# Kernel optimization log

Measured on AMD Instinct MI355X. Metric: run time of the kernel, lower is better.

The kernel has to match this reference:

```python
import jax, jax.numpy as jnp
import numpy as np

EPS = 1e-5
QMAX = 127.0


def fake_quant_int8(x):
    """Per-tensor symmetric int8 fake-quant (quantize+dequantize), dynamic scale.
    Mirrors brevitas Int8ActPerTensorFloat / Int8WeightPerTensorFloat math."""
    scale = jnp.maximum(jnp.max(jnp.abs(x)) / QMAX, 1e-8)
    q = jnp.clip(jnp.round(x / scale), -128.0, 127.0) * scale
    # straight-through estimator (identity grad through quant)
    return x + jax.lax.stop_gradient(q - x)


def layer_norm(x, g, b):
    mu = jnp.mean(x, axis=-1, keepdims=True)
    var = jnp.mean(jnp.square(x - mu), axis=-1, keepdims=True)
    return (x - mu) * jax.lax.rsqrt(var + EPS) * g + b


def setup_inputs() -> dict:
    key = jax.random.key(0)
    B, S, D, H = 64, 196, 768, 12
    M = 4 * D
    ks = jax.random.split(key, 8)
    s = lambda d: 1.0 / np.sqrt(d)
    return {
        "x": jax.random.normal(ks[0], (B, S, D), jnp.float32),
        "ln1_g": jnp.ones((D,), jnp.float32),
        "ln1_b": jnp.zeros((D,), jnp.float32),
        "ln2_g": jnp.ones((D,), jnp.float32),
        "ln2_b": jnp.zeros((D,), jnp.float32),
        "w_qkv": jax.random.normal(ks[1], (D, 3 * D), jnp.float32) * s(D),
        "b_qkv": jnp.zeros((3 * D,), jnp.float32),
        "w_o": jax.random.normal(ks[2], (D, D), jnp.float32) * s(D),
        "b_o": jnp.zeros((D,), jnp.float32),
        "w1": jax.random.normal(ks[3], (D, M), jnp.float32) * s(D),
        "b1": jnp.zeros((M,), jnp.float32),
        "w2": jax.random.normal(ks[4], (M, D), jnp.float32) * s(M),
        "b2": jnp.zeros((D,), jnp.float32),
    }


def _block(x, ln1_g, ln1_b, ln2_g, ln2_b, w_qkv, b_qkv, w_o, b_o, w1, b1, w2, b2):
    B, S, D = x.shape
    H = 12
    hd = D // H

    # --- LN -> quant -> MHSA -> add ---
    r1 = x
    h = fake_quant_int8(layer_norm(x, ln1_g, ln1_b))
    qkv = jnp.einsum("bsd,de->bse", h, fake_quant_int8(w_qkv)) + b_qkv
    q, k, v = jnp.split(qkv, 3, axis=-1)
    q = q.reshape(B, S, H, hd)
    k = k.reshape(B, S, H, hd)
    v = v.reshape(B, S, H, hd)
    logits = jnp.einsum("bqhd,bkhd->bhqk", q, k) / jnp.sqrt(jnp.float32(hd))
    attn = jax.nn.softmax(logits, axis=-1)
    ctx = jnp.einsum("bhqk,bkhd->bqhd", attn, v).reshape(B, S, D)
    ctx = fake_quant_int8(ctx)
    mhsa = jnp.einsum("bsd,de->bse", ctx, fake_quant_int8(w_o)) + b_o
    x = mhsa + r1

    # --- LN -> quant -> MLP (fc1 -> GELU -> quant -> fc2) -> add ---
    r2 = x
    h = fake_quant_int8(layer_norm(x, ln2_g, ln2_b))
    h = jnp.einsum("bsd,dm->bsm", h, fake_quant_int8(w1)) + b1
    h = jax.nn.gelu(h, approximate=False)  # torch nn.GELU default = exact erf
    h = fake_quant_int8(h)
    h = jnp.einsum("bsm,md->bsd", h, fake_quant_int8(w2)) + b2
    return h + r2


def reference(x, ln1_g, ln1_b, ln2_g, ln2_b, w_qkv, b_qkv, w_o, b_o, w1, b1, w2, b2):
    return _block(x, ln1_g, ln1_b, ln2_g, ln2_b, w_qkv, b_qkv, w_o, b_o, w1, b1, w2, b2)
```

## Files before the change

### kernel.cpp

```cpp
#include <hip/hip_runtime.h>
#include <cstdint>
#include <cstddef>

#define DEVFN __device__ __forceinline__

typedef short bf16x8 __attribute__((ext_vector_type(8)));
typedef float f32x4  __attribute__((ext_vector_type(4)));
typedef int   i32x4  __attribute__((ext_vector_type(4)));

static constexpr int NTOK  = 64 * 196;
static constexpr int DMODEL= 768;
static constexpr int NHEAD = 12;
static constexpr int NQKV  = 2304;
static constexpr int MMLP  = 3072;
static constexpr int SEQ   = 196;
static constexpr int NBATCH= 64;

enum { SL_LN1=0, SL_WQKV=1, SL_CTX=2, SL_WO=3, SL_LN2=4, SL_W1=5, SL_GELU=6, SL_W2=7 };

static constexpr int NSH       = 64;
static constexpr int SH_STRIDE = 64;
static constexpr int SLOTS_U32 = NSH * SH_STRIDE;

DEVFN float bf2f(unsigned short u){ return __uint_as_float(((unsigned)u) << 16); }
DEVFN unsigned short f2bf(float f){
  unsigned u = __float_as_uint(f);
  u += 0x7fffu + ((u >> 16) & 1u);
  return (unsigned short)(u >> 16);
}
DEVFN void split_bf(float v, unsigned short& hi, unsigned short& lo){
  hi = f2bf(v);
  lo = f2bf(v - bf2f(hi));
}
DEVFN float slot_absmax(const unsigned* __restrict__ slots, int slot){
  unsigned m = 0u;
#pragma unroll
  for (int j = 0; j < NSH; j++){
    unsigned u = slots[j * SH_STRIDE + slot];
    m = (u > m) ? u : m;
  }
  return __uint_as_float(m);
}
DEVFN float slot_scale(const unsigned* __restrict__ slots, int slot){
  return fmaxf(slot_absmax(slots, slot) / 127.0f, 1e-8f);
}
DEVFN void scatter_amax(unsigned* slots, int slot, unsigned bucket, float v){
  atomicMax(slots + (bucket & (NSH - 1)) * SH_STRIDE + slot, __float_as_uint(v));
}
DEVFN float quantval(float x, float s){
  float q = rintf(x / s);
  return fminf(fmaxf(q, -128.0f), 127.0f);
}
DEVFN unsigned pack4(float a, float b, float c, float d){
  return  ((unsigned)(unsigned char)(char)(int)a)
        | ((unsigned)(unsigned char)(char)(int)b << 8)
        | ((unsigned)(unsigned char)(char)(int)c << 16)
        | ((unsigned)(unsigned char)(char)(int)d << 24);
}
DEVFN float gelu_fast(float v){
  float s  = v * 0.70710678118654752f;
  float ax = fabsf(s);
  float t  = __builtin_amdgcn_rcpf(fmaf(0.3275911f, ax, 1.0f));
  float p  = t * fmaf(t, fmaf(t, fmaf(t, fmaf(t, 1.061405429f, -1.453152027f),
                                      1.421413741f), -0.284496736f), 0.254829592f);
  float er = fmaf(-p, __expf(-ax * ax), 1.0f);
  unsigned sgn = __float_as_uint(s) & 0x80000000u;
  er = __uint_as_float(__float_as_uint(er) | sgn);
  return 0.5f * v * (1.0f + er);
}
DEVFN f32x4 mfma16(bf16x8 a, bf16x8 b, f32x4 c){
  return __builtin_amdgcn_mfma_f32_16x16x32_bf16(a, b, c, 0, 0, 0);
}
DEVFN i32x4 mfma16i8(i32x4 a, i32x4 b, i32x4 c){
  return __builtin_amdgcn_mfma_i32_16x16x64_i8(a, b, c, 0, 0, 0);
}
DEVFN void async_ld16(const void* g, void* lds){
  __builtin_amdgcn_global_load_lds((const __attribute__((address_space(1))) void*)g,
                                   (__attribute__((address_space(3))) void*)lds, 16, 0, 0);
}
DEVFN int vidx(int d, int s){
  return d * 256 + (s ^ (((d ^ (d >> 2)) & 7) << 3));
}

__global__ void k_init(unsigned* slots){
  int i = blockIdx.x * blockDim.x + threadIdx.x;
  if (i < SLOTS_U32) slots[i] = 0u;
}

__global__ void k_absmax4(const float* __restrict__ x0, const float* __restrict__ x1,
                          const float* __restrict__ x2, const float* __restrict__ x3,
                          unsigned* slots){
  int bid = blockIdx.x;
  const float* x; int n4, slot, b0, nb;
  if (bid < 256)      { x = x0; n4 = DMODEL * NQKV  / 4; slot = SL_WQKV; b0 = 0;   nb = 256; }
  else if (bid < 384) { x = x1; n4 = DMODEL * DMODEL/ 4; slot = SL_WO;   b0 = 256; nb = 128; }
  else if (bid < 640) { x = x2; n4 = DMODEL * MMLP  / 4; slot = SL_W1;   b0 = 384; nb = 256; }
  else                { x = x3; n4 = MMLP   * DMODEL/ 4; slot = SL_W2;   b0 = 640; nb = 256; }
  int lb = bid - b0;
  float m = 0.f;
  const float4* x4 = (const float4*)x;
  int stride = nb * blockDim.x;
  for (int j = lb * blockDim.x + threadIdx.x; j < n4; j += stride){
    float4 v = x4[j];
    m = fmaxf(m, fmaxf(fmaxf(fabsf(v.x), fabsf(v.y)), fmaxf(fabsf(v.z), fabsf(v.w))));
  }
  for (int off = 32; off; off >>= 1) m = fmaxf(m, __shfl_xor(m, off));
  __shared__ float wm[4];
  int lane = threadIdx.x & 63, w = threadIdx.x >> 6;
  if (lane == 0) wm[w] = m;
  __syncthreads();
  if (threadIdx.x == 0){
    float bm = fmaxf(fmaxf(wm[0], wm[1]), fmaxf(wm[2], wm[3]));
    scatter_amax(slots, slot, bid, bm);
  }
}

__global__ void k_quant_transpose4(const float* __restrict__ w0, const float* __restrict__ w1,
                                   const float* __restrict__ w2, const float* __restrict__ w3,
                                   char* __restrict__ t0, char* __restrict__ t1,
                                   char* __restrict__ t2, char* __restrict__ t3,
                                   const unsigned* __restrict__ slots){
  int bid = blockIdx.x;
  const float* w; char* wt; int K, N, slot, lb;
  if (bid < 1728)      { w = w0; wt = t0; K = DMODEL; N = NQKV;   slot = SL_WQKV; lb = bid; }
  else if (bid < 2304) { w = w1; wt = t1; K = DMODEL; N = DMODEL; slot = SL_WO;   lb = bid - 1728; }
  else if (bid < 4608) { w = w2; wt = t2; K = DMODEL; N = MMLP;   slot = SL_W1;   lb = bid - 2304; }
  else                 { w = w3; wt = t3; K = MMLP;   N = DMODEL; slot = SL_W2;   lb = bid - 4608; }
  int nx = N / 32;
  int bx = lb % nx, by = lb / nx;

  __shared__ float tile[32][33];
  float s = slot_scale(slots, slot);
  int n0 = bx * 32, k0 = by * 32;
  int tx = threadIdx.x & 31, ty = threadIdx.x >> 5;
#pragma unroll
  for (int i = 0; i < 4; i++){
    int k = k0 + ty + i * 8;
    float v = w[(size_t)k * N + n0 + tx];
    tile[ty + i * 8][tx] = quantval(v, s);
  }
  __syncthreads();
  int n = threadIdx.x >> 3, kg = threadIdx.x & 7;
  unsigned o = pack4(tile[kg * 4 + 0][n], tile[kg * 4 + 1][n],
                     tile[kg * 4 + 2][n], tile[kg * 4 + 3][n]);
  *(unsigned*)(wt + (size_t)(n0 + n) * K + k0 + kg * 4) = o;
}

__global__ void k_layernorm(const float* __restrict__ x, const float* __restrict__ g,
                            const float* __restrict__ b, float* __restrict__ out,
                            unsigned* slots, int slot){
  int w = threadIdx.x >> 6, lane = threadIdx.x & 63;
  int row = blockIdx.x * 4 + w;
  const float4* xr = (const float4*)(x + (size_t)row * DMODEL);
  float4 v[3];
  float sum = 0.f;
#pragma unroll
  for (int i = 0; i < 3; i++){ v[i] = xr[i * 64 + lane]; sum += v[i].x + v[i].y + v[i].z + v[i].w; }
  for (int off = 32; off; off >>= 1) sum += __shfl_xor(sum, off);
  float mu = sum * (1.0f / 768.0f);
  float vs = 0.f;
#pragma unroll
  for (int i = 0; i < 3; i++){
    float dx = v[i].x - mu, dy = v[i].y - mu, dz = v[i].z - mu, dw = v[i].w - mu;
    vs += dx * dx + dy * dy + dz * dz + dw * dw;
  }
  for (int off = 32; off; off >>= 1) vs += __shfl_xor(vs, off);
  float inv = 1.0f / sqrtf(vs * (1.0f / 768.0f) + 1e-5f);
  const float4* g4 = (const float4*)g; const float4* b4 = (const float4*)b;
  float4* o4 = (float4*)(out + (size_t)row * DMODEL);
  float am = 0.f;
#pragma unroll
  for (int i = 0; i < 3; i++){
    float4 gg = g4[i * 64 + lane], bb = b4[i * 64 + lane], o;
    o.x = (v[i].x - mu) * inv * gg.x + bb.x;
    o.y = (v[i].y - mu) * inv * gg.y + bb.y;
    o.z = (v[i].z - mu) * inv * gg.z + bb.z;
    o.w = (v[i].w - mu) * inv * gg.w + bb.w;
    am = fmaxf(am, fmaxf(fmaxf(fabsf(o.x), fabsf(o.y)), fmaxf(fabsf(o.z), fabsf(o.w))));
    o4[i * 64 + lane] = o;
  }
  for (int off = 32; off; off >>= 1) am = fmaxf(am, __shfl_xor(am, off));
  __shared__ float am4[4];
  if (lane == 0) am4[w] = am;
  __syncthreads();
  if (threadIdx.x == 0){
    float bm = fmaxf(fmaxf(am4[0], am4[1]), fmaxf(am4[2], am4[3]));
    scatter_amax(slots, slot, blockIdx.x, bm);
  }
}

__global__ void k_quant_act(const float* __restrict__ x, unsigned* __restrict__ out,
                            int n4, const unsigned* __restrict__ slots, int slot){
  float s = slot_scale(slots, slot);
  const float4* x4 = (const float4*)x;
  int stride = gridDim.x * blockDim.x;
  for (int j = blockIdx.x * blockDim.x + threadIdx.x; j < n4; j += stride){
    float4 v = x4[j];
    out[j] = pack4(quantval(v.x, s), quantval(v.y, s), quantval(v.z, s), quantval(v.w, s));
  }
}

__global__ void k_quant_bf16_i8(const unsigned short* __restrict__ x, unsigned* __restrict__ out,
                                int n4, const unsigned* __restrict__ slots, int slot){
  float s = slot_scale(slots, slot);
  const ushort4* x4 = (const ushort4*)x;
  int stride = gridDim.x * blockDim.x;
  for (int j = blockIdx.x * blockDim.x + threadIdx.x; j < n4; j += stride){
    ushort4 v = x4[j];
    out[j] = pack4(quantval(bf2f(v.x), s), quantval(bf2f(v.y), s),
                   quantval(bf2f(v.z), s), quantval(bf2f(v.w), s));
  }
}

template<int EPI>
__launch_bounds__(256, 4)
__global__ void k_gemm(const char* __restrict__ A,
                       const char* __restrict__ Bt,
                       const float* __restrict__ bias,
                       const float* __restrict__ res,
                       float* __restrict__ Cf,
                       unsigned short* __restrict__ Cb,
                       const unsigned* __restrict__ slots, int sa_slot, int sb_slot,
                       unsigned* gmax_slots, int gmax_slot,
                       int M, int N, int K)
{
  __shared__ __align__(16) char smem[32768];
  __shared__ float gm4[4];
  const int tid  = threadIdx.x;
  const int lane = tid & 63;
  const int wv   = tid >> 6;
  const int wx   = wv & 1, wy = wv >> 1;
  const int quad = lane >> 4;
  const int l16  = lane & 15;
  const int m0 = blockIdx.y * 128, n0 = blockIdx.x * 128;

  auto issue = [&](int k0, int buf){
#pragma unroll
    for (int i = 0; i < 2; i++){
      int c = tid + i * 256;
      int row = c >> 2, q = c & 3;
      int qs = (q - ((row + (row >> 2)) & 3)) & 3;
      async_ld16(A + (size_t)(m0 + row) * K + k0 + qs * 16,
                 smem + buf * 8192 + (i * 256 + wv * 64) * 16);
    }
#pragma unroll
    for (int i = 0; i < 2; i++){
      int c = tid + i * 256;
      int row = c >> 2, q = c & 3;
      int qs = (q - ((row + (row >> 2)) & 3)) & 3;
      async_ld16(Bt + (size_t)(n0 + row) * K + k0 + qs * 16,
                 smem + 16384 + buf * 8192 + (i * 256 + wv * 64) * 16);
    }
  };

  i32x4 acc[4][4] = {};
  const int nk = K >> 6;
  issue(0, 0);

  const int ch = (((quad + (l16 & 3) + (l16 >> 2)) & 3)) * 16;

  for (int k = 0; k < nk; k++){
    const int cur = k & 1;
    if (k + 1 < nk){
      issue((k + 1) << 6, cur ^ 1);
      asm volatile("s_waitcnt vmcnt(4)" ::: "memory");
    } else {
      asm volatile("s_waitcnt vmcnt(0)" ::: "memory");
    }
    asm volatile("s_barrier" ::: "memory");

    const char* Ab = smem + cur * 8192;
    const char* Bb = smem + 16384 + cur * 8192;
    i32x4 af[4], bfr[4];
#pragma unroll
    for (int i = 0; i < 4; i++)
      af[i] = *(const i32x4*)(Ab + (wy * 64 + i * 16 + l16) * 64 + ch);
#pragma unroll
    for (int j = 0; j < 4; j++)
      bfr[j] = *(const i32x4*)(Bb + (wx * 64 + j * 16 + l16) * 64 + ch);
    asm volatile("s_waitcnt lgkmcnt(0)" ::: "memory");
    asm volatile("s_barrier" ::: "memory");

#pragma unroll
    for (int i = 0; i < 4; i++)
#pragma unroll
      for (int j = 0; j < 4; j++)
        acc[i][j] = mfma16i8(af[i], bfr[j], acc[i][j]);
  }
  __syncthreads();

  float (*stage)[132] = (float (*)[132])smem;
  const float sc = slot_scale(slots, sa_slot) * slot_scale(slots, sb_slot);
  const int col4 = (tid & 31) * 4;
  const int gc   = n0 + col4;
  const float4 bb = *(const float4*)&bias[gc];
  float gmax = 0.f;
#pragma unroll
  for (int i = 0; i < 4; i++){
#pragma unroll
    for (int j = 0; j < 4; j++)
#pragma unroll
      for (int r = 0; r < 4; r++)
        stage[wy * 16 + quad * 4 + r][wx * 64 + j * 16 + l16] = (float)acc[i][j][r];
    __syncthreads();
#pragma unroll
    for (int rr = 0; rr < 4; rr++){
      const int rl = rr * 8 + (tid >> 5);
      const int gm = m0 + ((rl >> 4) * 64) + i * 16 + (rl & 15);
      float4 v = *(const float4*)&stage[rl][col4];
      v.x = v.x * sc + bb.x; v.y = v.y * sc + bb.y;
      v.z = v.z * sc + bb.z; v.w = v.w * sc + bb.w;
      if constexpr (EPI == 1){
        float4 rv = *(const float4*)&res[(size_t)gm * N + gc];
        v.x += rv.x; v.y += rv.y; v.z += rv.z; v.w += rv.w;
        *(float4*)&Cf[(size_t)gm * N + gc] = v;
      } else if constexpr (EPI == 2){
        float g0 = gelu_fast(v.x);
        float g1 = gelu_fast(v.y);
        float g2 = gelu_fast(v.z);
        float g3 = gelu_fast(v.w);
        gmax = fmaxf(gmax, fmaxf(fmaxf(fabsf(g0), fabsf(g1)), fmaxf(fabsf(g2), fabsf(g3))));
        ushort4 o = {f2bf(g0), f2bf(g1), f2bf(g2), f2bf(g3)};
        *(ushort4*)&Cb[(size_t)gm * N + gc] = o;
      } else {
        *(float4*)&Cf[(size_t)gm * N + gc] = v;
      }
    }
    __syncthreads();
  }
  if constexpr (EPI == 2){
    for (int off = 32; off; off >>= 1) gmax = fmaxf(gmax, __shfl_xor(gmax, off));
    if (lane == 0) gm4[wv] = gmax;
    __syncthreads();
    if (tid == 0){
      float bm = fmaxf(fmaxf(gm4[0], gm4[1]), fmaxf(gm4[2], gm4[3]));
      scatter_amax(gmax_slots, gmax_slot, blockIdx.x + blockIdx.y * gridDim.x, bm);
    }
  }
}

__launch_bounds__(832, 4)
__global__ void k_attention(const float* __restrict__ qkv, float* __restrict__ ctx,
                            unsigned* slots){
  __shared__ __align__(16) unsigned short Khi[208 * 72], Klo[208 * 72];
  __shared__ __align__(16) unsigned short Vhi[64 * 256], Vlo[64 * 256];
  __shared__ __align__(16) unsigned short Ps[13][2][16 * 40];
  __shared__ float gm[13];

  const int bh = blockIdx.x;
  const int b = bh / NHEAD, h = bh % NHEAD;
  const float* base = qkv + (size_t)b * SEQ * NQKV;
  const int tid = threadIdx.x, lane = tid & 63, wv = tid >> 6;
  const int quad = lane >> 4, l16 = lane & 15;

  float4 kreg[4], vreg[5];
#pragma unroll
  for (int i = 0; i < 4; i++){
    int idx = tid + i * 832;
    int r = idx >> 4, c4 = (idx & 15) * 4;
    float4 v = {0.f, 0.f, 0.f, 0.f};
    if (r < SEQ) v = *(const float4*)(base + (size_t)r * NQKV + DMODEL + h * 64 + c4);
    kreg[i] = v;
  }
#pragma unroll
  for (int i = 0; i < 5; i++){
    int idx = tid + i * 832;
    int s = idx >> 4, dg = (idx & 15) * 4;
    float4 v = {0.f, 0.f, 0.f, 0.f};
    if (idx < 232 * 16 && s < SEQ)
      v = *(const float4*)(base + (size_t)s * NQKV + 2 * DMODEL + h * 64 + dg);
    vreg[i] = v;
  }
#pragma unroll
  for (int i = 0; i < 4; i++){
    int idx = tid + i * 832;
    int r = idx >> 4, c4 = (idx & 15) * 4;
    float4 v = kreg[i];
    unsigned short h0,l0,h1,l1,h2,l2,h3,l3;
    split_bf(v.x, h0, l0); split_bf(v.y, h1, l1); split_bf(v.z, h2, l2); split_bf(v.w, h3, l3);
    ushort4 hs = {h0, h1, h2, h3}, ls = {l0, l1, l2, l3};
    *(ushort4*)(Khi + r * 72 + c4) = hs;
    *(ushort4*)(Klo + r * 72 + c4) = ls;
  }
#pragma unroll
  for (int i = 0; i < 5; i++){
    int idx = tid + i * 832;
    if (idx < 232 * 16){
      int s = idx >> 4, dg = (idx & 15) * 4;
      float4 v = vreg[i];
      unsigned short hi, lo;
      split_bf(v.x, hi, lo); Vhi[vidx(dg + 0, s)] = hi; Vlo[vidx(dg + 0, s)] = lo;
      split_bf(v.y, hi, lo); Vhi[vidx(dg + 1, s)] = hi; Vlo[vidx(dg + 1, s)] = lo;
      split_bf(v.z, hi, lo); Vhi[vidx(dg + 2, s)] = hi; Vlo[vidx(dg + 2, s)] = lo;
      split_bf(v.w, hi, lo); Vhi[vidx(dg + 3, s)] = hi; Vlo[vidx(dg + 3, s)] = lo;
    }
  }
  __syncthreads();

  unsigned short* PsH = &Ps[wv][0][0];
  unsigned short* PsL = &Ps[wv][1][0];

  float gmax = 0.f;
  const int qt = wv;
  {
    const int q0 = qt * 16;
    const int sq = q0 + l16;
    const bool valid = sq < SEQ;

    bf16x8 aqh[2], aql[2];
    const float* qrow = base + (size_t)(valid ? sq : 0) * NQKV + h * 64;
#pragma unroll
    for (int ks = 0; ks < 2; ks++){
      float4 v0 = {0,0,0,0}, v1 = {0,0,0,0};
      if (valid){
        v0 = *(const float4*)(qrow + ks * 32 + quad * 8);
        v1 = *(const float4*)(qrow + ks * 32 + quad * 8 + 4);
      }
      float vv[8] = {v0.x, v0.y, v0.z, v0.w, v1.x, v1.y, v1.z, v1.w};
#pragma unroll
      for (int j = 0; j < 8; j++){
        unsigned short hi, lo; split_bf(vv[j], hi, lo);
        aqh[ks][j] = (short)hi; aql[ks][j] = (short)lo;
      }
    }

    f32x4 sacc[13];
    __builtin_amdgcn_s_setprio(1);
#pragma unroll
    for (int t = 0; t < 13; t++){
      f32x4 a = {0.f, 0.f, 0.f, 0.f};
#pragma unroll
      for (int ks = 0; ks < 2; ks++){
        bf16x8 bkh = *(const bf16x8*)(Khi + (t * 16 + l16) * 72 + ks * 32 + quad * 8);
        bf16x8 bkl = *(const bf16x8*)(Klo + (t * 16 + l16) * 72 + ks * 32 + quad * 8);
        a = mfma16(aqh[ks], bkh, a);
        a = mfma16(aqh[ks], bkl, a);
        a = mfma16(aql[ks], bkh, a);
      }
      sacc[t] = a;
    }
    __builtin_amdgcn_s_setprio(0);

    float mx[4] = {-1e30f, -1e30f, -1e30f, -1e30f};
#pragma unroll
    for (int t = 0; t < 13; t++){
      bool dead = (t == 12) && (l16 >= 4);
#pragma unroll
      for (int r = 0; r < 4; r++){
        float v = dead ? -1e30f : sacc[t][r] * 0.125f;
        sacc[t][r] = v;
        mx[r] = fmaxf(mx[r], v);
      }
    }
#pragma unroll
    for (int off = 1; off < 16; off <<= 1)
#pragma unroll
      for (int r = 0; r < 4; r++) mx[r] = fmaxf(mx[r], __shfl_xor(mx[r], off));
    float sum[4] = {0.f, 0.f, 0.f, 0.f};
#pragma unroll
    for (int t = 0; t < 13; t++)
#pragma unroll
      for (int r = 0; r < 4; r++){
        float e = __expf(sacc[t][r] - mx[r]);
        sacc[t][r] = e; sum[r] += e;
      }
#pragma unroll
    for (int off = 1; off < 16; off <<= 1)
#pragma unroll
      for (int r = 0; r < 4; r++) sum[r] += __shfl_xor(sum[r], off);
    float inv[4];
#pragma unroll
    for (int r = 0; r < 4; r++) inv[r] = 1.0f / sum[r];

    f32x4 oacc[4] = {};
#pragma unroll
    for (int ks = 0; ks < 7; ks++){
      const int t0 = 2 * ks, t1 = 2 * ks + 1;
#pragma unroll
      for (int r = 0; r < 4; r++){
        int row = quad * 4 + r;
        unsigned short hi, lo;
        split_bf(sacc[t0][r] * inv[r], hi, lo);
        PsH[row * 40 + l16] = hi; PsL[row * 40 + l16] = lo;
        if (t1 < 13){
          split_bf(sacc[t1][r] * inv[r], hi, lo);
          PsH[row * 40 + 16 + l16] = hi; PsL[row * 40 + 16 + l16] = lo;
        } else {
          PsH[row * 40 + 16 + l16] = 0; PsL[row * 40 + 16 + l16] = 0;
        }
      }
      __builtin_amdgcn_wave_barrier();
      bf16x8 aph = *(const bf16x8*)(PsH + l16 * 40 + quad * 8);
      bf16x8 apl = *(const bf16x8*)(PsL + l16 * 40 + quad * 8);
      __builtin_amdgcn_s_setprio(1);
#pragma unroll
      for (int n = 0; n < 4; n++){
        bf16x8 bvh = *(const bf16x8*)(Vhi + vidx(n * 16 + l16, ks * 32 + quad * 8));
        bf16x8 bvl = *(const bf16x8*)(Vlo + vidx(n * 16 + l16, ks * 32 + quad * 8));
        oacc[n] = mfma16(aph, bvh, oacc[n]);
        oacc[n] = mfma16(aph, bvl, oacc[n]);
        oacc[n] = mfma16(apl, bvh, oacc[n]);
      }
      __builtin_amdgcn_s_setprio(0);
      __builtin_amdgcn_wave_barrier();
    }

#pragma unroll
    for (int r = 0; r < 4; r++){
      int srow = q0 + quad * 4 + r;
      if (srow < SEQ){
#pragma unroll
        for (int n = 0; n < 4; n++){
          float v = oacc[n][r];
          ctx[((size_t)(b * SEQ + srow)) * DMODEL + h * 64 + n * 16 + l16] = v;
          gmax = fmaxf(gmax, fabsf(v));
        }
      }
    }
  }
  for (int off = 32; off; off >>= 1) gmax = fmaxf(gmax, __shfl_xor(gmax, off));
  if (lane == 0) gm[wv] = gmax;
  __syncthreads();
  if (tid == 0){
    float bm = 0.f;
#pragma unroll
    for (int i = 0; i < 13; i++) bm = fmaxf(bm, gm[i]);
    scatter_amax(slots, SL_CTX, blockIdx.x, bm);
  }
}

extern "C" void kernel_launch(void* const* d_in, const int* in_sizes, int n_in,
                              void* d_out, int out_size, void* d_ws, size_t ws_size,
                              hipStream_t stream)
{
  const float* x     = (const float*)d_in[0];
  const float* ln1_g = (const float*)d_in[1];
  const float* ln1_b = (const float*)d_in[2];
  const float* ln2_g = (const float*)d_in[3];
  const float* ln2_b = (const float*)d_in[4];
  const float* w_qkv = (const float*)d_in[5];
  const float* b_qkv = (const float*)d_in[6];
  const float* w_o   = (const float*)d_in[7];
  const float* b_o   = (const float*)d_in[8];
  const float* w1    = (const float*)d_in[9];
  const float* b1    = (const float*)d_in[10];
  const float* w2    = (const float*)d_in[11];
  const float* b2    = (const float*)d_in[12];

  char* ws = (char*)d_ws;
  size_t off = 0;
  unsigned* slots = (unsigned*)ws;                 off += SLOTS_U32 * 4;
  char* wqkvT = (char*)(ws + off); off += (size_t)NQKV  * DMODEL;
  char* woT   = (char*)(ws + off); off += (size_t)DMODEL* DMODEL;
  char* w1T   = (char*)(ws + off); off += (size_t)MMLP  * DMODEL;
  char* w2T   = (char*)(ws + off); off += (size_t)DMODEL* MMLP;
  off = (off + 255) & ~(size_t)255;
  float* t1    = (float*)(ws + off);               off += (size_t)NTOK * DMODEL * 4;
  char*  t1q   = (char*)(ws + off);                off += (size_t)NTOK * DMODEL;
  off = (off + 255) & ~(size_t)255;
  float* qkv   = (float*)(ws + off);               off += (size_t)NTOK * NQKV * 4;
  float* xmid  = (float*)(ws + off);               off += (size_t)NTOK * DMODEL * 4;
  unsigned short* h1 = (unsigned short*)qkv;
  char* h1q = (char*)qkv + (size_t)NTOK * MMLP * 2;
  float* outp = (float*)d_out;

  k_init<<<(SLOTS_U32 + 255) / 256, 256, 0, stream>>>(slots);

  k_absmax4<<<896, 256, 0, stream>>>(w_qkv, w_o, w1, w2, slots);

  k_quant_transpose4<<<6912, 256, 0, stream>>>(w_qkv, w_o, w1, w2,
                                               wqkvT, woT, w1T, w2T, slots);

  k_layernorm<<<NTOK / 4, 256, 0, stream>>>(x, ln1_g, ln1_b, t1, slots, SL_LN1);
  {
    int n4 = NTOK * DMODEL / 4;
    k_quant_act<<<2048, 256, 0, stream>>>(t1, (unsigned*)t1q, n4, slots, SL_LN1);
  }
  k_gemm<0><<<dim3(NQKV / 128, NTOK / 128), 256, 0, stream>>>(
      t1q, wqkvT, b_qkv, nullptr, qkv, nullptr, slots, SL_LN1, SL_WQKV, nullptr, 0,
      NTOK, NQKV, DMODEL);

  k_attention<<<NBATCH * NHEAD, 832, 0, stream>>>(qkv, t1, slots);
  {
    int n4 = NTOK * DMODEL / 4;
    k_quant_act<<<2048, 256, 0, stream>>>(t1, (unsigned*)t1q, n4, slots, SL_CTX);
  }
  k_gemm<1><<<dim3(DMODEL / 128, NTOK / 128), 256, 0, stream>>>(
      t1q, woT, b_o, x, xmid, nullptr, slots, SL_CTX, SL_WO, nullptr, 0,
      NTOK, DMODEL, DMODEL);

  k_layernorm<<<NTOK / 4, 256, 0, stream>>>(xmid, ln2_g, ln2_b, t1, slots, SL_LN2);
  {
    int n4 = NTOK * DMODEL / 4;
    k_quant_act<<<2048, 256, 0, stream>>>(t1, (unsigned*)t1q, n4, slots, SL_LN2);
  }
  k_gemm<2><<<dim3(MMLP / 128, NTOK / 128), 256, 0, stream>>>(
      t1q, w1T, b1, nullptr, nullptr, h1, slots, SL_LN2, SL_W1, slots, SL_GELU,
      NTOK, MMLP, DMODEL);
  {
    int n4 = NTOK * MMLP / 4;
    k_quant_bf16_i8<<<2048, 256, 0, stream>>>(h1, (unsigned*)h1q, n4, slots, SL_GELU);
  }
  k_gemm<1><<<dim3(DMODEL / 128, NTOK / 128), 256, 0, stream>>>(
      h1q, w2T, b2, xmid, outp, nullptr, slots, SL_GELU, SL_W2, nullptr, 0,
      NTOK, DMODEL, MMLP);
}
```

Baseline: 468.0 us.

## Use packed hardware bf16 conversion and XCD-aware block swizzle in GEMM

Replaces the software round-to-nearest-even float-to-bf16 conversion with the v_cvt_pk_bf16_f32 instruction, which converts two values per op. The hi/lo split used for the emulated-fp32 attention matmuls and the GELU epilogue store now use it. Separately, GEMM block indices are remapped so that consecutive tiles land on the same XCD, aiming to improve L2 reuse of A/B tiles. Hardware rounding should match RNE for finite values, but NaN handling may differ.

```diff
diff --git a/kernel.cpp b/kernel.cpp
--- a/kernel.cpp
+++ b/kernel.cpp
@@ -23,14 +23,16 @@
 static constexpr int SLOTS_U32 = NSH * SH_STRIDE;
 
 DEVFN float bf2f(unsigned short u){ return __uint_as_float(((unsigned)u) << 16); }
-DEVFN unsigned short f2bf(float f){
-  unsigned u = __float_as_uint(f);
-  u += 0x7fffu + ((u >> 16) & 1u);
-  return (unsigned short)(u >> 16);
-}
-DEVFN void split_bf(float v, unsigned short& hi, unsigned short& lo){
-  hi = f2bf(v);
-  lo = f2bf(v - bf2f(hi));
+DEVFN unsigned cvt_pk_bf16(float a, float b){
+  unsigned r;
+  asm("v_cvt_pk_bf16_f32 %0, %1, %2" : "=v"(r) : "v"(a), "v"(b));
+  return r;
+}
+DEVFN void split_pk(float a, float b, unsigned& hp, unsigned& lp){
+  hp = cvt_pk_bf16(a, b);
+  float ra = a - __uint_as_float(hp << 16);
+  float rb = b - __uint_as_float(hp & 0xffff0000u);
+  lp = cvt_pk_bf16(ra, rb);
 }
 DEVFN float slot_absmax(const unsigned* __restrict__ slots, int slot){
   unsigned m = 0u;
@@ -80,6 +82,14 @@
 }
 DEVFN int vidx(int d, int s){
   return d * 256 + (s ^ (((d ^ (d >> 2)) & 7) << 3));
+}
+DEVFN void xcd_swizzle(int gx, int gy, int& bx, int& by){
+  int nwg = gx * gy;
+  int bid = blockIdx.y * gx + blockIdx.x;
+  int q = nwg >> 3, r = nwg & 7;
+  int xcd = bid & 7, loc = bid >> 3;
+  int sw = (xcd < r) ? (xcd * (q + 1) + loc) : (r * (q + 1) + (xcd - r) * q + loc);
+  bx = sw % gx; by = sw / gx;
 }
 
 __global__ void k_init(unsigned* slots){
@@ -232,7 +242,9 @@
   const int wx   = wv & 1, wy = wv >> 1;
   const int quad = lane >> 4;
   const int l16  = lane & 15;
-  const int m0 = blockIdx.y * 128, n0 = blockIdx.x * 128;
+  int bx, by;
+  xcd_swizzle(gridDim.x, gridDim.y, bx, by);
+  const int m0 = by * 128, n0 = bx * 128;
 
   auto issue = [&](int k0, int buf){
 #pragma unroll
@@ -320,8 +332,8 @@
         float g2 = gelu_fast(v.z);
         float g3 = gelu_fast(v.w);
         gmax = fmaxf(gmax, fmaxf(fmaxf(fabsf(g0), fabsf(g1)), fmaxf(fabsf(g2), fabsf(g3))));
-        ushort4 o = {f2bf(g0), f2bf(g1), f2bf(g2), f2bf(g3)};
-        *(ushort4*)&Cb[(size_t)gm * N + gc] = o;
+        uint2 o = {cvt_pk_bf16(g0, g1), cvt_pk_bf16(g2, g3)};
+        *(uint2*)&Cb[(size_t)gm * N + gc] = o;
       } else {
         *(float4*)&Cf[(size_t)gm * N + gc] = v;
       }
@@ -376,11 +388,11 @@
     int idx = tid + i * 832;
     int r = idx >> 4, c4 = (idx & 15) * 4;
     float4 v = kreg[i];
-    unsigned short h0,l0,h1,l1,h2,l2,h3,l3;
-    split_bf(v.x, h0, l0); split_bf(v.y, h1, l1); split_bf(v.z, h2, l2); split_bf(v.w, h3, l3);
-    ushort4 hs = {h0, h1, h2, h3}, ls = {l0, l1, l2, l3};
-    *(ushort4*)(Khi + r * 72 + c4) = hs;
-    *(ushort4*)(Klo + r * 72 + c4) = ls;
+    unsigned h01, l01, h23, l23;
+    split_pk(v.x, v.y, h01, l01);
+    split_pk(v.z, v.w, h23, l23);
+    *(uint2*)(Khi + r * 72 + c4) = uint2{h01, h23};
+    *(uint2*)(Klo + r * 72 + c4) = uint2{l01, l23};
   }
 #pragma unroll
   for (int i = 0; i < 5; i++){
@@ -388,11 +400,13 @@
     if (idx < 232 * 16){
       int s = idx >> 4, dg = (idx & 15) * 4;
       float4 v = vreg[i];
-      unsigned short hi, lo;
-      split_bf(v.x, hi, lo); Vhi[vidx(dg + 0, s)] = hi; Vlo[vidx(dg + 0, s)] = lo;
-      split_bf(v.y, hi, lo); Vhi[vidx(dg + 1, s)] = hi; Vlo[vidx(dg + 1, s)] = lo;
-      split_bf(v.z, hi, lo); Vhi[vidx(dg + 2, s)] = hi; Vlo[vidx(dg + 2, s)] = lo;
-      split_bf(v.w, hi, lo); Vhi[vidx(dg + 3, s)] = hi; Vlo[vidx(dg + 3, s)] = lo;
+      unsigned h01, l01, h23, l23;
+      split_pk(v.x, v.y, h01, l01);
+      split_pk(v.z, v.w, h23, l23);
+      Vhi[vidx(dg + 0, s)] = (unsigned short)h01; Vhi[vidx(dg + 1, s)] = (unsigned short)(h01 >> 16);
+      Vhi[vidx(dg + 2, s)] = (unsigned short)h23; Vhi[vidx(dg + 3, s)] = (unsigned short)(h23 >> 16);
+      Vlo[vidx(dg + 0, s)] = (unsigned short)l01; Vlo[vidx(dg + 1, s)] = (unsigned short)(l01 >> 16);
+      Vlo[vidx(dg + 2, s)] = (unsigned short)l23; Vlo[vidx(dg + 3, s)] = (unsigned short)(l23 >> 16);
     }
   }
   __syncthreads();
@@ -416,12 +430,12 @@
         v0 = *(const float4*)(qrow + ks * 32 + quad * 8);
         v1 = *(const float4*)(qrow + ks * 32 + quad * 8 + 4);
       }
-      float vv[8] = {v0.x, v0.y, v0.z, v0.w, v1.x, v1.y, v1.z, v1.w};
-#pragma unroll
-      for (int j = 0; j < 8; j++){
-        unsigned short hi, lo; split_bf(vv[j], hi, lo);
-        aqh[ks][j] = (short)hi; aql[ks][j] = (short)lo;
-      }
+      unsigned* ah = (unsigned*)&aqh[ks];
+      unsigned* al = (unsigned*)&aql[ks];
+      split_pk(v0.x, v0.y, ah[0], al[0]);
+      split_pk(v0.z, v0.w, ah[1], al[1]);
+      split_pk(v1.x, v1.y, ah[2], al[2]);
+      split_pk(v1.z, v1.w, ah[3], al[3]);
     }
 
     f32x4 sacc[13];
@@ -479,15 +493,14 @@
 #pragma unroll
       for (int r = 0; r < 4; r++){
         int row = quad * 4 + r;
-        unsigned short hi, lo;
-        split_bf(sacc[t0][r] * inv[r], hi, lo);
-        PsH[row * 40 + l16] = hi; PsL[row * 40 + l16] = lo;
-        if (t1 < 13){
-          split_bf(sacc[t1][r] * inv[r], hi, lo);
-          PsH[row * 40 + 16 + l16] = hi; PsL[row * 40 + 16 + l16] = lo;
-        } else {
-          PsH[row * 40 + 16 + l16] = 0; PsL[row * 40 + 16 + l16] = 0;
-        }
+        float a = sacc[t0][r] * inv[r];
+        float c = (t1 < 13) ? sacc[t1][r] * inv[r] : 0.f;
+        unsigned hp, lp;
+        split_pk(a, c, hp, lp);
+        PsH[row * 40 + l16]      = (unsigned short)hp;
+        PsH[row * 40 + 16 + l16] = (unsigned short)(hp >> 16);
+        PsL[row * 40 + l16]      = (unsigned short)lp;
+        PsL[row * 40 + 16 + l16] = (unsigned short)(lp >> 16);
       }
       __builtin_amdgcn_wave_barrier();
       bf16x8 aph = *(const bf16x8*)(PsH + l16 * 40 + quad * 8);
```

Measured after the change: 443.5 us. 5.2% less time.
